# Kernel tuning notes

Measured on AMD Instinct MI355X. Metric: run time of the kernel, lower is better.

## Reference

```python
import jax, jax.numpy as jnp
import numpy as np
import math

B, T, C, H, E = 1, 384, 512, 8, 16
D = C // H

def layer_norm(x, w, b, eps=1e-5):
    mu = jnp.mean(x, axis=-1, keepdims=True)
    var = jnp.mean(jnp.square(x - mu), axis=-1, keepdims=True)
    return (x - mu) * jax.lax.rsqrt(var + eps) * w + b

def setup_inputs() -> dict:
    key = jax.random.key(0)
    ks = jax.random.split(key, 12)
    s = 0.02
    return {
        'x': jax.random.normal(ks[0], (B, T, C), jnp.float32),
        'bias_matrix': jax.random.randint(ks[1], (B, T, T), 0, E, jnp.int32),
        'ln1_w': jnp.ones((C,), jnp.float32),
        'ln1_b': jnp.zeros((C,), jnp.float32),
        'w_attn_w': jax.random.normal(ks[2], (3 * C, C), jnp.float32) * s,
        'w_attn_b': jnp.zeros((3 * C,), jnp.float32),
        'w_proj_w': jax.random.normal(ks[3], (C, C), jnp.float32) * s,
        'w_proj_b': jnp.zeros((C,), jnp.float32),
        'attn_bias_emb': jax.random.normal(ks[4], (E, H), jnp.float32) * s,
        'edge_emb': jax.random.normal(ks[5], (E, C), jnp.float32) * s,
        'w_edge_k_w': jax.random.normal(ks[6], (C, C), jnp.float32) * s,
        'w_edge_k_b': jnp.zeros((C,), jnp.float32),
        'w_edge_v_w': jax.random.normal(ks[7], (C, C), jnp.float32) * s,
        'w_edge_v_b': jnp.zeros((C,), jnp.float32),
        'ln2_w': jnp.ones((C,), jnp.float32),
        'ln2_b': jnp.zeros((C,), jnp.float32),
        'c_fc_w': jax.random.normal(ks[8], (4 * C, C), jnp.float32) * s,
        'c_fc_b': jnp.zeros((4 * C,), jnp.float32),
        'c_proj_w': jax.random.normal(ks[9], (C, 4 * C), jnp.float32) * s,
        'c_proj_b': jnp.zeros((C,), jnp.float32),
    }

def reference(x, bias_matrix, ln1_w, ln1_b, w_attn_w, w_attn_b, w_proj_w, w_proj_b,
              attn_bias_emb, edge_emb, w_edge_k_w, w_edge_k_b, w_edge_v_w, w_edge_v_b,
              ln2_w, ln2_b, c_fc_w, c_fc_b, c_proj_w, c_proj_b):
    # --- attention branch ---
    h = layer_norm(x, ln1_w, ln1_b)
    qkv = h @ w_attn_w.T + w_attn_b                      # (B,T,3C)
    q, k, v = jnp.split(qkv, 3, axis=-1)
    q = q.reshape(B, T, H, D).transpose(0, 2, 1, 3)      # (B,H,T,D)
    k = k.reshape(B, T, H, D).transpose(0, 2, 1, 3)
    v = v.reshape(B, T, H, D).transpose(0, 2, 1, 3)
    scale = math.sqrt(D)

    ee = edge_emb[bias_matrix]                           # (B,T,T,C)
    e_k = (ee @ w_edge_k_w.T + w_edge_k_b).reshape(B, T, T, H, D)
    # score[b,h,i,j] = sum_d q[b,h,i,d] * k[b,h,j,d] * e_k[b,i,j,h,d]
    scores = jnp.einsum('bhid,bhjd,bijhd->bhij', q, k, e_k) / scale

    mask = jnp.tril(jnp.ones((T, T), bool))              # causal, diag included
    scores = jnp.where(mask, scores, -jnp.inf)
    ab = attn_bias_emb[bias_matrix].transpose(0, 3, 1, 2)  # (B,H,T,T)
    ab = jnp.where(mask, ab, 0.0)
    attn = jax.nn.softmax(scores + ab, axis=-1)

    e_v = (ee @ w_edge_v_w.T + w_edge_v_b).reshape(B, T, T, H, D)
    # y[b,h,i,d] = sum_j attn[b,h,i,j] * v[b,h,j,d] * e_v[b,i,j,h,d]
    y = jnp.einsum('bhij,bhjd,bijhd->bhid', attn, v, e_v)
    y = y.transpose(0, 2, 1, 3).reshape(B, T, C)
    y = y @ w_proj_w.T + w_proj_b
    x = x + y

    # --- MLP branch ---
    h2 = layer_norm(x, ln2_w, ln2_b)
    h2 = jax.nn.gelu(h2 @ c_fc_w.T + c_fc_b, approximate=False)
    x = x + (h2 @ c_proj_w.T + c_proj_b)
    return x
```

## Files before the change

### kernel.cpp

```cpp
#include <hip/hip_runtime.h>
#include <math.h>

#define TT 384
#define CC 512
#define HH 8
#define EE 16

typedef __bf16 bf16_t;
typedef __bf16 bf16x8 __attribute__((ext_vector_type(8)));
typedef __bf16 bf16x4v __attribute__((ext_vector_type(4)));
typedef float f32x4 __attribute__((ext_vector_type(4)));

__device__ __forceinline__ float wave_reduce_sum(float v) {
#pragma unroll
  for (int off = 32; off >= 1; off >>= 1) v += __shfl_xor(v, off, 64);
  return v;
}

__device__ __forceinline__ void wrow_unit(const float* __restrict__ wr,
                                          const float* __restrict__ g,
                                          const float* __restrict__ bb,
                                          float extra_c, bf16_t* __restrict__ orow,
                                          float* __restrict__ s1p,
                                          float* __restrict__ cp, int lane) {
  const float* p = wr + lane * 8;
  f32x4 w0 = *(const f32x4*)p, w1 = *(const f32x4*)(p + 4);
  f32x4 g0 = *(const f32x4*)(g + lane * 8), g1 = *(const f32x4*)(g + lane * 8 + 4);
  f32x4 b0 = *(const f32x4*)(bb + lane * 8), b1 = *(const f32x4*)(bb + lane * 8 + 4);
  f32x4 p0 = w0 * g0, p1 = w1 * g1;
  bf16x8 o;
  o[0] = (bf16_t)p0.x; o[1] = (bf16_t)p0.y; o[2] = (bf16_t)p0.z; o[3] = (bf16_t)p0.w;
  o[4] = (bf16_t)p1.x; o[5] = (bf16_t)p1.y; o[6] = (bf16_t)p1.z; o[7] = (bf16_t)p1.w;
  *(bf16x8*)(orow + lane * 8) = o;
  float s1 = p0.x + p0.y + p0.z + p0.w + p1.x + p1.y + p1.z + p1.w;
  float c = w0.x * b0.x + w0.y * b0.y + w0.z * b0.z + w0.w * b0.w +
            w1.x * b1.x + w1.y * b1.y + w1.z * b1.z + w1.w * b1.w;
  s1 = wave_reduce_sum(s1);
  c = wave_reduce_sum(c);
  if (lane == 0) { *s1p = s1; *cp = c + extra_c; }
}

struct PreArgs {
  const float *x, *ln1w, *ln1b, *wattn, *wattnb, *eemb, *wekw, *wekb, *wevw,
      *wevb, *ln2w, *ln2b, *cfcw, *cfcb, *wproj, *wcproj;
  float *ektab, *evtab, *xmu, *xrs, *x1s1, *x1s2, *s1q, *cq, *s1f, *cf;
  bf16_t *wqkv_bf, *wfc_bf, *wproj_bf, *wcproj_bf;
};

__global__ __launch_bounds__(256) void pre_k(PreArgs P) {
  int b = blockIdx.x, tid = threadIdx.x, lane = tid & 63, wave = tid >> 6;
  if (b < 256) {
    int wid = b * 4 + wave;
    int gbase = wid * 16;
    int table = gbase >> 13;
    int e = (gbase >> 9) & 15;
    int c0 = gbase & 511;
    const float* er = P.eemb + e * 512 + lane * 8;
    f32x4 ea = *(const f32x4*)er;
    f32x4 eb = *(const f32x4*)(er + 4);
    const float* wbase = table ? P.wevw : P.wekw;
    const float* bbase = table ? P.wevb : P.wekb;
    float* obase = (table ? P.evtab : P.ektab) + e * 512;
#pragma unroll
    for (int o = 0; o < 16; o++) {
      int c = c0 + o;
      const float* wr = wbase + (size_t)c * 512 + lane * 8;
      f32x4 wa = *(const f32x4*)wr;
      f32x4 wb = *(const f32x4*)(wr + 4);
      float acc = ea.x * wa.x + ea.y * wa.y + ea.z * wa.z + ea.w * wa.w +
                  eb.x * wb.x + eb.y * wb.y + eb.z * wb.z + eb.w * wb.w;
      acc = wave_reduce_sum(acc);
      if (lane == 0) obase[c] = acc + bbase[c];
    }
  } else if (b < 640) {
    int n = (b - 256) * 4 + wave;
    wrow_unit(P.wattn + (size_t)n * 512, P.ln1w, P.ln1b, P.wattnb[n],
              P.wqkv_bf + (size_t)n * 512, P.s1q + n, P.cq + n, lane);
  } else if (b < 1152) {
    int n = (b - 640) * 4 + wave;
    wrow_unit(P.cfcw + (size_t)n * 512, P.ln2w, P.ln2b, P.cfcb[n],
              P.wfc_bf + (size_t)n * 512, P.s1f + n, P.cf + n, lane);
  } else if (b < 1216) {
    int base = (b - 1152) * 1024;
    for (int u = tid; u < 1024; u += 256) {
      f32x4 a = *((const f32x4*)P.wproj + base + u);
      bf16x4v o;
      o[0] = (bf16_t)a.x; o[1] = (bf16_t)a.y; o[2] = (bf16_t)a.z; o[3] = (bf16_t)a.w;
      *((bf16x4v*)P.wproj_bf + base + u) = o;
    }
  } else if (b < 1472) {
    int base = (b - 1216) * 1024;
    for (int u = tid; u < 1024; u += 256) {
      f32x4 a = *((const f32x4*)P.wcproj + base + u);
      bf16x4v o;
      o[0] = (bf16_t)a.x; o[1] = (bf16_t)a.y; o[2] = (bf16_t)a.z; o[3] = (bf16_t)a.w;
      *((bf16x4v*)P.wcproj_bf + base + u) = o;
    }
  } else if (b < 1568) {
    int r = (b - 1472) * 4 + wave;
    const float* xr = P.x + (size_t)r * 512 + lane * 8;
    f32x4 a = *(const f32x4*)xr, c = *(const f32x4*)(xr + 4);
    float s = a.x + a.y + a.z + a.w + c.x + c.y + c.z + c.w;
    float q = a.x * a.x + a.y * a.y + a.z * a.z + a.w * a.w +
              c.x * c.x + c.y * c.y + c.z * c.z + c.w * c.w;
    s = wave_reduce_sum(s);
    q = wave_reduce_sum(q);
    if (lane == 0) {
      float mu = s * (1.0f / 512.0f);
      float var = q * (1.0f / 512.0f) - mu * mu;
      P.xmu[r] = mu;
      P.xrs[r] = rsqrtf(var + 1e-5f);
    }
  } else {
    for (int i = tid; i < 384; i += 256) { P.x1s1[i] = 0.f; P.x1s2[i] = 0.f; }
  }
}

template <int MODE>
__global__ __launch_bounds__(256) void gemm_k(
    const void* __restrict__ Aptr, const bf16_t* __restrict__ Wb,
    const float* __restrict__ e0, const float* __restrict__ e1,
    const float* __restrict__ e2, const float* __restrict__ e3,
    const float* __restrict__ res, void* __restrict__ out,
    float* __restrict__ st1, float* __restrict__ st2, int N, int K) {
  constexpr bool AF32 = (MODE == 0 || MODE == 2);
  constexpr int AW = AF32 ? 2 : 1;
  __shared__ float part[4][32][32];
  int tid = threadIdx.x;
  int lane = tid & 63, wave = tid >> 6;
  int m0 = blockIdx.y * 32, n0 = blockIdx.x * 32;
  int r16 = lane & 15, quad = lane >> 4;
  int kchunk = K >> 2, k0 = wave * kchunk;

  f32x4 acc[2][2];
  f32x4 zero = {0.f, 0.f, 0.f, 0.f};
#pragma unroll
  for (int i = 0; i < 2; i++)
#pragma unroll
    for (int j = 0; j < 2; j++) acc[i][j] = zero;

  const float* Af = (const float*)Aptr + (size_t)(m0 + r16) * K + k0 + quad * 8;
  const bf16_t* Ab = (const bf16_t*)Aptr + (size_t)(m0 + r16) * K + k0 + quad * 8;
  const bf16_t* Wp = Wb + (size_t)(n0 + r16) * K + k0 + quad * 8;

  for (int kb0 = 0; kb0 < kchunk; kb0 += 128) {
    uint4 araw[4][2][AW];
    uint4 braw[4][2];
#pragma unroll
    for (int u = 0; u < 4; u++) {
      int kb = kb0 + u * 32;
#pragma unroll
      for (int t = 0; t < 2; t++) {
        if (AF32) {
          araw[u][t][0] = *(const uint4*)(Af + (size_t)t * 16 * K + kb);
          araw[u][t][1] = *(const uint4*)(Af + (size_t)t * 16 * K + kb + 4);
        } else {
          araw[u][t][0] = *(const uint4*)(Ab + (size_t)t * 16 * K + kb);
        }
        braw[u][t] = *(const uint4*)(Wp + (size_t)t * 16 * K + kb);
      }
    }
#pragma unroll
    for (int u = 0; u < 4; u++) {
      bf16x8 af[2], bfr[2];
#pragma unroll
      for (int t = 0; t < 2; t++) {
        if (AF32) {
          f32x4 a = *reinterpret_cast<const f32x4*>(&araw[u][t][0]);
          f32x4 c = *reinterpret_cast<const f32x4*>(&araw[u][t][1]);
          af[t][0] = (bf16_t)a.x; af[t][1] = (bf16_t)a.y;
          af[t][2] = (bf16_t)a.z; af[t][3] = (bf16_t)a.w;
          af[t][4] = (bf16_t)c.x; af[t][5] = (bf16_t)c.y;
          af[t][6] = (bf16_t)c.z; af[t][7] = (bf16_t)c.w;
        } else {
          af[t] = *reinterpret_cast<const bf16x8*>(&araw[u][t][0]);
        }
        bfr[t] = *reinterpret_cast<const bf16x8*>(&braw[u][t]);
      }
#pragma unroll
      for (int i = 0; i < 2; i++)
#pragma unroll
        for (int j = 0; j < 2; j++)
          acc[i][j] = __builtin_amdgcn_mfma_f32_16x16x32_bf16(af[i], bfr[j],
                                                              acc[i][j], 0, 0, 0);
    }
  }

#pragma unroll
  for (int i = 0; i < 2; i++)
#pragma unroll
    for (int j = 0; j < 2; j++)
#pragma unroll
      for (int r = 0; r < 4; r++)
        part[wave][i * 16 + quad * 4 + r][j * 16 + r16] = acc[i][j][r];
  __syncthreads();

  int row = tid >> 3, c4 = (tid & 7) * 4;
  f32x4 v = *(const f32x4*)&part[0][row][c4];
  v += *(const f32x4*)&part[1][row][c4];
  v += *(const f32x4*)&part[2][row][c4];
  v += *(const f32x4*)&part[3][row][c4];
  int grow = m0 + row, gcol = n0 + c4;

  if (MODE == 0 || MODE == 2) {
    float mu, rs;
    if (MODE == 0) {
      mu = e0[grow]; rs = e1[grow];
    } else {
      float S = e0[grow], Q = e1[grow];
      mu = S * (1.0f / 512.0f);
      float var = Q * (1.0f / 512.0f) - mu * mu;
      rs = rsqrtf(var + 1e-5f);
    }
    f32x4 s1v = *(const f32x4*)(e2 + gcol);
    f32x4 ccv = *(const f32x4*)(e3 + gcol);
#pragma unroll
    for (int t = 0; t < 4; t++) {
      float x = rs * (v[t] - mu * s1v[t]) + ccv[t];
      if (MODE == 2) x = 0.5f * x * (1.0f + erff(x * 0.70710678118654752f));
      v[t] = x;
    }
    bf16x4v o;
#pragma unroll
    for (int t = 0; t < 4; t++) o[t] = (bf16_t)v[t];
    *(bf16x4v*)((bf16_t*)out + (size_t)grow * N + gcol) = o;
  } else {
    v += *(const f32x4*)(e2 + gcol);
    v += *(const f32x4*)(res + (size_t)grow * N + gcol);
    *(f32x4*)((float*)out + (size_t)grow * N + gcol) = v;
    if (MODE == 1) {
      float sv = v.x + v.y + v.z + v.w;
      float qv = v.x * v.x + v.y * v.y + v.z * v.z + v.w * v.w;
      sv += __shfl_down(sv, 4, 8); qv += __shfl_down(qv, 4, 8);
      sv += __shfl_down(sv, 2, 8); qv += __shfl_down(qv, 2, 8);
      sv += __shfl_down(sv, 1, 8); qv += __shfl_down(qv, 1, 8);
      if ((tid & 7) == 0) {
        atomicAdd(st1 + grow, sv);
        atomicAdd(st2 + grow, qv);
      }
    }
  }
}

__global__ __launch_bounds__(256) void attn_k(
    const bf16_t* __restrict__ qkv, const int* __restrict__ bias_matrix,
    const float* __restrict__ attn_bias_emb, const float* __restrict__ ek_tab,
    const float* __restrict__ ev_tab, bf16_t* __restrict__ ybuf) {
  __shared__ float s[TT];
  __shared__ int ebuf[TT];
  __shared__ float qe[EE][68];
  __shared__ float evh[EE * 64];
  __shared__ float red[4 * 64];
  __shared__ float absh[EE];
  __shared__ float scr[4];

  int i = blockIdx.x, h = blockIdx.y;
  int tid = threadIdx.x, lane = tid & 63, wave = tid >> 6;
  int n = i + 1;

  for (int j = tid; j < n; j += 256) ebuf[j] = bias_matrix[i * TT + j];
  if (tid < EE) absh[tid] = attn_bias_emb[tid * HH + h];
  for (int idx = tid; idx < EE * 64; idx += 256) {
    int e = idx >> 6, d = idx & 63;
    float qv = (float)qkv[(size_t)i * 1536 + h * 64 + d];
    qe[e][d] = qv * ek_tab[e * 512 + h * 64 + d];
    evh[idx] = ev_tab[e * 512 + h * 64 + d];
  }
  __syncthreads();

  float ls = 0.0f;
  for (int jl = tid; jl < n; jl += 256) {
    int e = ebuf[jl];
    const uint4* kp = (const uint4*)(qkv + (size_t)jl * 1536 + 512 + h * 64);
    uint4 kr[8];
#pragma unroll
    for (int dg = 0; dg < 8; dg++) kr[dg] = kp[dg];
    float acc = 0.f;
#pragma unroll
    for (int dg = 0; dg < 8; dg++) {
      bf16x8 kv = *reinterpret_cast<const bf16x8*>(&kr[dg]);
      f32x4 qa = *(const f32x4*)&qe[e][dg * 8];
      f32x4 qb = *(const f32x4*)&qe[e][dg * 8 + 4];
      acc += (float)kv[0] * qa.x + (float)kv[1] * qa.y + (float)kv[2] * qa.z +
             (float)kv[3] * qa.w + (float)kv[4] * qb.x + (float)kv[5] * qb.y +
             (float)kv[6] * qb.z + (float)kv[7] * qb.w;
    }
    float p = __expf(acc * 0.125f + absh[e]);
    s[jl] = p;
    ls += p;
  }
  ls = wave_reduce_sum(ls);
  if (lane == 0) scr[wave] = ls;
  __syncthreads();
  float inv = 1.0f / (scr[0] + scr[1] + scr[2] + scr[3]);

  float acc = 0.0f;
  int j = wave;
  for (; j + 4 < n; j += 8) {
    int e0 = ebuf[j], e1 = ebuf[j + 4];
    float p0 = s[j], p1 = s[j + 4];
    float v0 = (float)qkv[(size_t)j * 1536 + 1024 + h * 64 + lane];
    float v1 = (float)qkv[(size_t)(j + 4) * 1536 + 1024 + h * 64 + lane];
    acc += p0 * v0 * evh[e0 * 64 + lane] + p1 * v1 * evh[e1 * 64 + lane];
  }
  for (; j < n; j += 4) {
    int e = ebuf[j];
    float vv = (float)qkv[(size_t)j * 1536 + 1024 + h * 64 + lane];
    acc += s[j] * vv * evh[e * 64 + lane];
  }
  red[wave * 64 + lane] = acc;
  __syncthreads();
  if (tid < 64) {
    float y = (red[tid] + red[64 + tid] + red[128 + tid] + red[192 + tid]) * inv;
    ybuf[(size_t)i * CC + h * 64 + tid] = (bf16_t)y;
  }
}

extern "C" void kernel_launch(void* const* d_in, const int* in_sizes, int n_in,
                              void* d_out, int out_size, void* d_ws,
                              size_t ws_size, hipStream_t stream) {
  const float* x = (const float*)d_in[0];
  const int* bias_mat = (const int*)d_in[1];

  char* wp = (char*)d_ws;
  float* ektab = (float*)wp;  wp += 16 * 512 * 4;
  float* evtab = (float*)wp;  wp += 16 * 512 * 4;
  float* xmu = (float*)wp;    wp += 384 * 4;
  float* xrs = (float*)wp;    wp += 384 * 4;
  float* x1s1 = (float*)wp;   wp += 384 * 4;
  float* x1s2 = (float*)wp;   wp += 384 * 4;
  float* s1q = (float*)wp;    wp += 1536 * 4;
  float* cq = (float*)wp;     wp += 1536 * 4;
  float* s1f = (float*)wp;    wp += 2048 * 4;
  float* cf = (float*)wp;     wp += 2048 * 4;
  float* x1 = (float*)wp;     wp += 384 * 512 * 4;
  bf16_t* wqkv_bf = (bf16_t*)wp;   wp += 1536 * 512 * 2;
  bf16_t* wfc_bf = (bf16_t*)wp;    wp += 2048 * 512 * 2;
  bf16_t* wproj_bf = (bf16_t*)wp;  wp += 512 * 512 * 2;
  bf16_t* wcproj_bf = (bf16_t*)wp; wp += 512 * 2048 * 2;
  bf16_t* qkv = (bf16_t*)wp;  wp += 384 * 1536 * 2;
  bf16_t* ybuf = (bf16_t*)wp; wp += 384 * 512 * 2;
  bf16_t* gbuf = (bf16_t*)wp; wp += 384 * 2048 * 2;

  PreArgs P;
  P.x = x;
  P.ln1w = (const float*)d_in[2];
  P.ln1b = (const float*)d_in[3];
  P.wattn = (const float*)d_in[4];
  P.wattnb = (const float*)d_in[5];
  P.eemb = (const float*)d_in[9];
  P.wekw = (const float*)d_in[10];
  P.wekb = (const float*)d_in[11];
  P.wevw = (const float*)d_in[12];
  P.wevb = (const float*)d_in[13];
  P.ln2w = (const float*)d_in[14];
  P.ln2b = (const float*)d_in[15];
  P.cfcw = (const float*)d_in[16];
  P.cfcb = (const float*)d_in[17];
  P.wproj = (const float*)d_in[6];
  P.wcproj = (const float*)d_in[18];
  P.ektab = ektab; P.evtab = evtab; P.xmu = xmu; P.xrs = xrs;
  P.x1s1 = x1s1; P.x1s2 = x1s2; P.s1q = s1q; P.cq = cq; P.s1f = s1f; P.cf = cf;
  P.wqkv_bf = wqkv_bf; P.wfc_bf = wfc_bf; P.wproj_bf = wproj_bf;
  P.wcproj_bf = wcproj_bf;

  pre_k<<<1569, 256, 0, stream>>>(P);
  gemm_k<0><<<dim3(48, 12), 256, 0, stream>>>(x, wqkv_bf, xmu, xrs, s1q, cq,
                                              nullptr, qkv, nullptr, nullptr,
                                              1536, 512);
  attn_k<<<dim3(TT, HH), 256, 0, stream>>>(qkv, bias_mat,
                                           (const float*)d_in[8], ektab, evtab,
                                           ybuf);
  gemm_k<1><<<dim3(16, 12), 256, 0, stream>>>(
      ybuf, wproj_bf, nullptr, nullptr, (const float*)d_in[7], nullptr, x, x1,
      x1s1, x1s2, 512, 512);
  gemm_k<2><<<dim3(64, 12), 256, 0, stream>>>(x1, wfc_bf, x1s1, x1s2, s1f, cf,
                                              nullptr, gbuf, nullptr, nullptr,
                                              2048, 512);
  gemm_k<3><<<dim3(16, 12), 256, 0, stream>>>(
      gbuf, wcproj_bf, nullptr, nullptr, (const float*)d_in[19], nullptr, x1,
      d_out, nullptr, nullptr, 512, 2048);
}
```

Baseline: 173.9 us.

## Move weight/table prep off critical path into extra blocks of QKV GEMM

The pre-kernel now handles only the work the QKV GEMM depends on: converting the QKV weights and computing the LN1 row stats. The edge K/V tables, fc/proj weight conversions and fc row sums are done by 1088 extra blocks appended to the QKV GEMM grid (grid y raised from 12 to 35). This shortens the serial pre-kernel and overlaps the independent prep with the GEMM. The cost is a larger GEMM grid and a branch at GEMM entry; the added blocks may contend with GEMM blocks for CUs and bandwidth.

```diff
diff --git a/kernel.cpp b/kernel.cpp
--- a/kernel.cpp
+++ b/kernel.cpp
@@ -40,27 +40,28 @@
   if (lane == 0) { *s1p = s1; *cp = c + extra_c; }
 }
 
-struct PreArgs {
-  const float *x, *ln1w, *ln1b, *wattn, *wattnb, *eemb, *wekw, *wekb, *wevw,
-      *wevb, *ln2w, *ln2b, *cfcw, *cfcb, *wproj, *wcproj;
-  float *ektab, *evtab, *xmu, *xrs, *x1s1, *x1s2, *s1q, *cq, *s1f, *cf;
-  bf16_t *wqkv_bf, *wfc_bf, *wproj_bf, *wcproj_bf;
+struct PrepX {
+  const float *eemb, *wekw, *wekb, *wevw, *wevb;
+  const float *ln2w, *ln2b, *cfcw, *cfcb;
+  const float *wproj, *wcproj;
+  float *ektab, *evtab, *s1f, *cf;
+  bf16_t *wfc_bf, *wproj_bf, *wcproj_bf;
 };
 
-__global__ __launch_bounds__(256) void pre_k(PreArgs P) {
-  int b = blockIdx.x, tid = threadIdx.x, lane = tid & 63, wave = tid >> 6;
-  if (b < 256) {
-    int wid = b * 4 + wave;
+__device__ void prep_unit(int u, const PrepX& X, int tid) {
+  int lane = tid & 63, wave = tid >> 6;
+  if (u < 256) {
+    int wid = u * 4 + wave;
     int gbase = wid * 16;
     int table = gbase >> 13;
     int e = (gbase >> 9) & 15;
     int c0 = gbase & 511;
-    const float* er = P.eemb + e * 512 + lane * 8;
+    const float* er = X.eemb + e * 512 + lane * 8;
     f32x4 ea = *(const f32x4*)er;
     f32x4 eb = *(const f32x4*)(er + 4);
-    const float* wbase = table ? P.wevw : P.wekw;
-    const float* bbase = table ? P.wevb : P.wekb;
-    float* obase = (table ? P.evtab : P.ektab) + e * 512;
+    const float* wbase = table ? X.wevw : X.wekw;
+    const float* bbase = table ? X.wevb : X.wekb;
+    float* obase = (table ? X.evtab : X.ektab) + e * 512;
 #pragma unroll
     for (int o = 0; o < 16; o++) {
       int c = c0 + o;
@@ -72,32 +73,43 @@
       acc = wave_reduce_sum(acc);
       if (lane == 0) obase[c] = acc + bbase[c];
     }
-  } else if (b < 640) {
-    int n = (b - 256) * 4 + wave;
+  } else if (u < 768) {
+    int n = (u - 256) * 4 + wave;
+    wrow_unit(X.cfcw + (size_t)n * 512, X.ln2w, X.ln2b, X.cfcb[n],
+              X.wfc_bf + (size_t)n * 512, X.s1f + n, X.cf + n, lane);
+  } else if (u < 1024) {
+    int base = (u - 768) * 1024;
+    for (int t = tid; t < 1024; t += 256) {
+      f32x4 a = *((const f32x4*)X.wcproj + base + t);
+      bf16x4v o;
+      o[0] = (bf16_t)a.x; o[1] = (bf16_t)a.y; o[2] = (bf16_t)a.z; o[3] = (bf16_t)a.w;
+      *((bf16x4v*)X.wcproj_bf + base + t) = o;
+    }
+  } else if (u < 1088) {
+    int base = (u - 1024) * 1024;
+    for (int t = tid; t < 1024; t += 256) {
+      f32x4 a = *((const f32x4*)X.wproj + base + t);
+      bf16x4v o;
+      o[0] = (bf16_t)a.x; o[1] = (bf16_t)a.y; o[2] = (bf16_t)a.z; o[3] = (bf16_t)a.w;
+      *((bf16x4v*)X.wproj_bf + base + t) = o;
+    }
+  }
+}
+
+struct PreArgs {
+  const float *x, *ln1w, *ln1b, *wattn, *wattnb;
+  float *xmu, *xrs, *x1s1, *x1s2, *s1q, *cq;
+  bf16_t* wqkv_bf;
+};
+
+__global__ __launch_bounds__(256) void pre_k(PreArgs P) {
+  int b = blockIdx.x, tid = threadIdx.x, lane = tid & 63, wave = tid >> 6;
+  if (b < 384) {
+    int n = b * 4 + wave;
     wrow_unit(P.wattn + (size_t)n * 512, P.ln1w, P.ln1b, P.wattnb[n],
               P.wqkv_bf + (size_t)n * 512, P.s1q + n, P.cq + n, lane);
-  } else if (b < 1152) {
-    int n = (b - 640) * 4 + wave;
-    wrow_unit(P.cfcw + (size_t)n * 512, P.ln2w, P.ln2b, P.cfcb[n],
-              P.wfc_bf + (size_t)n * 512, P.s1f + n, P.cf + n, lane);
-  } else if (b < 1216) {
-    int base = (b - 1152) * 1024;
-    for (int u = tid; u < 1024; u += 256) {
-      f32x4 a = *((const f32x4*)P.wproj + base + u);
-      bf16x4v o;
-      o[0] = (bf16_t)a.x; o[1] = (bf16_t)a.y; o[2] = (bf16_t)a.z; o[3] = (bf16_t)a.w;
-      *((bf16x4v*)P.wproj_bf + base + u) = o;
-    }
-  } else if (b < 1472) {
-    int base = (b - 1216) * 1024;
-    for (int u = tid; u < 1024; u += 256) {
-      f32x4 a = *((const f32x4*)P.wcproj + base + u);
-      bf16x4v o;
-      o[0] = (bf16_t)a.x; o[1] = (bf16_t)a.y; o[2] = (bf16_t)a.z; o[3] = (bf16_t)a.w;
-      *((bf16x4v*)P.wcproj_bf + base + u) = o;
-    }
-  } else if (b < 1568) {
-    int r = (b - 1472) * 4 + wave;
+  } else if (b < 480) {
+    int r = (b - 384) * 4 + wave;
     const float* xr = P.x + (size_t)r * 512 + lane * 8;
     f32x4 a = *(const f32x4*)xr, c = *(const f32x4*)(xr + 4);
     float s = a.x + a.y + a.z + a.w + c.x + c.y + c.z + c.w;
@@ -122,11 +134,15 @@
     const float* __restrict__ e0, const float* __restrict__ e1,
     const float* __restrict__ e2, const float* __restrict__ e3,
     const float* __restrict__ res, void* __restrict__ out,
-    float* __restrict__ st1, float* __restrict__ st2, int N, int K) {
+    float* __restrict__ st1, float* __restrict__ st2, int N, int K, PrepX X) {
   constexpr bool AF32 = (MODE == 0 || MODE == 2);
   constexpr int AW = AF32 ? 2 : 1;
   __shared__ float part[4][32][32];
   int tid = threadIdx.x;
+  if (MODE == 0 && blockIdx.y >= 12) {
+    prep_unit((blockIdx.y - 12) * gridDim.x + blockIdx.x, X, tid);
+    return;
+  }
   int lane = tid & 63, wave = tid >> 6;
   int m0 = blockIdx.y * 32, n0 = blockIdx.x * 32;
   int r16 = lane & 15, quad = lane >> 4;
@@ -348,36 +364,38 @@
   P.ln1b = (const float*)d_in[3];
   P.wattn = (const float*)d_in[4];
   P.wattnb = (const float*)d_in[5];
-  P.eemb = (const float*)d_in[9];
-  P.wekw = (const float*)d_in[10];
-  P.wekb = (const float*)d_in[11];
-  P.wevw = (const float*)d_in[12];
-  P.wevb = (const float*)d_in[13];
-  P.ln2w = (const float*)d_in[14];
-  P.ln2b = (const float*)d_in[15];
-  P.cfcw = (const float*)d_in[16];
-  P.cfcb = (const float*)d_in[17];
-  P.wproj = (const float*)d_in[6];
-  P.wcproj = (const float*)d_in[18];
-  P.ektab = ektab; P.evtab = evtab; P.xmu = xmu; P.xrs = xrs;
-  P.x1s1 = x1s1; P.x1s2 = x1s2; P.s1q = s1q; P.cq = cq; P.s1f = s1f; P.cf = cf;
-  P.wqkv_bf = wqkv_bf; P.wfc_bf = wfc_bf; P.wproj_bf = wproj_bf;
-  P.wcproj_bf = wcproj_bf;
-
-  pre_k<<<1569, 256, 0, stream>>>(P);
-  gemm_k<0><<<dim3(48, 12), 256, 0, stream>>>(x, wqkv_bf, xmu, xrs, s1q, cq,
+  P.xmu = xmu; P.xrs = xrs; P.x1s1 = x1s1; P.x1s2 = x1s2;
+  P.s1q = s1q; P.cq = cq; P.wqkv_bf = wqkv_bf;
+
+  PrepX X;
+  X.eemb = (const float*)d_in[9];
+  X.wekw = (const float*)d_in[10];
+  X.wekb = (const float*)d_in[11];
+  X.wevw = (const float*)d_in[12];
+  X.wevb = (const float*)d_in[13];
+  X.ln2w = (const float*)d_in[14];
+  X.ln2b = (const float*)d_in[15];
+  X.cfcw = (const float*)d_in[16];
+  X.cfcb = (const float*)d_in[17];
+  X.wproj = (const float*)d_in[6];
+  X.wcproj = (const float*)d_in[18];
+  X.ektab = ektab; X.evtab = evtab; X.s1f = s1f; X.cf = cf;
+  X.wfc_bf = wfc_bf; X.wproj_bf = wproj_bf; X.wcproj_bf = wcproj_bf;
+
+  pre_k<<<481, 256, 0, stream>>>(P);
+  gemm_k<0><<<dim3(48, 35), 256, 0, stream>>>(x, wqkv_bf, xmu, xrs, s1q, cq,
                                               nullptr, qkv, nullptr, nullptr,
-                                              1536, 512);
+                                              1536, 512, X);
   attn_k<<<dim3(TT, HH), 256, 0, stream>>>(qkv, bias_mat,
                                            (const float*)d_in[8], ektab, evtab,
                                            ybuf);
   gemm_k<1><<<dim3(16, 12), 256, 0, stream>>>(
       ybuf, wproj_bf, nullptr, nullptr, (const float*)d_in[7], nullptr, x, x1,
-      x1s1, x1s2, 512, 512);
+      x1s1, x1s2, 512, 512, X);
   gemm_k<2><<<dim3(64, 12), 256, 0, stream>>>(x1, wfc_bf, x1s1, x1s2, s1f, cf,
                                               nullptr, gbuf, nullptr, nullptr,
-                                              2048, 512);
+                                              2048, 512, X);
   gemm_k<3><<<dim3(16, 12), 256, 0, stream>>>(
       gbuf, wcproj_bf, nullptr, nullptr, (const float*)d_in[19], nullptr, x1,
-      d_out, nullptr, nullptr, 512, 2048);
-}
+      d_out, nullptr, nullptr, 512, 2048, X);
+}
```

Result: no change. 174.8 us (+0.6%).
